# Kernel optimization log

Measured on AMD Instinct MI355X. Metric: run time of the kernel, lower is better.

Reference implementation:

```python
import jax, jax.numpy as jnp
import numpy as np


def setup_inputs() -> dict:
    key = jax.random.key(0)
    ks = jax.random.split(key, 8)
    H, O, B, T = 1024, 512, 512, 256
    s_ih = 1.0 / np.sqrt(H)
    return {
        "h0": jax.random.normal(ks[0], (1, B, H), jnp.float32),
        "c0": jax.random.normal(ks[1], (1, B, H), jnp.float32),
        "W_ih": jax.random.normal(ks[2], (4 * H, O), jnp.float32) * s_ih,
        "W_hh": jax.random.normal(ks[3], (4 * H, H), jnp.float32) * s_ih,
        "b_ih": jax.random.normal(ks[4], (4 * H,), jnp.float32) * s_ih,
        "b_hh": jax.random.normal(ks[5], (4 * H,), jnp.float32) * s_ih,
        "W_out": jax.random.normal(ks[6], (O, H), jnp.float32) * s_ih,
        "b_out": jax.random.normal(ks[7], (O,), jnp.float32) * s_ih,
        "out_len": T,
    }


def reference(h0, c0, W_ih, W_hh, b_ih, b_hh, W_out, b_out, out_len):
    B = h0.shape[1]
    O = W_out.shape[0]
    h = h0.reshape(B, -1)  # [B, H]
    c = c0.reshape(B, -1)  # [B, H]
    x = jnp.zeros((B, O), dtype=h.dtype)  # initial lstm_in of zeros

    def step(carry, _):
        h, c, x = carry
        # PyTorch LSTMCell: gates ordered (i, f, g, o)
        gates = x @ W_ih.T + b_ih + h @ W_hh.T + b_hh  # [B, 4H]
        i, f, g, o = jnp.split(gates, 4, axis=-1)
        c_new = jax.nn.sigmoid(f) * c + jax.nn.sigmoid(i) * jnp.tanh(g)
        h_new = jax.nn.sigmoid(o) * jnp.tanh(c_new)
        y = jax.nn.softmax(h_new @ W_out.T + b_out, axis=-1)  # [B, O]
        return (h_new, c_new, y), y

    _, ys = jax.lax.scan(step, (h, c, x), None, length=out_len)
    # original writes output[i-1] for i = out_len..1, i.e. time-reversed storage
    return ys[::-1]  # [out_len, B, O]
```

## Files before the change

### kernel.cpp

```cpp
#include <hip/hip_runtime.h>
#include <math.h>

#define BB 512
#define HH 1024
#define OO 512
#define KC 1536
#define G4H 4096
#define TT 256

typedef _Float16 half8 __attribute__((ext_vector_type(8)));
typedef float f32x4 __attribute__((ext_vector_type(4)));

__device__ __forceinline__ void dma16(const void* g, void* l) {
    __builtin_amdgcn_global_load_lds(
        (const __attribute__((address_space(1))) void*)g,
        (__attribute__((address_space(3))) void*)l, 16, 0, 0);
}

__global__ __launch_bounds__(256) void conv_wcat(
    const float* __restrict__ W_ih, const float* __restrict__ W_hh,
    _Float16* __restrict__ Wcat)
{
    int k = blockIdx.x * 256 + threadIdx.x;
    int p = blockIdx.y;
    int g = (p >> 5) & 3, jt = p >> 7, jr = p & 31;
    int n = g * HH + jt * 32 + jr;
    float v = (k < OO) ? W_ih[(size_t)n * OO + k] : W_hh[(size_t)n * HH + (k - OO)];
    Wcat[(size_t)p * KC + k] = (_Float16)v;
}

__global__ __launch_bounds__(256) void conv_wout(
    const float* __restrict__ W_out, _Float16* __restrict__ Wout16)
{
    int k = blockIdx.x * 256 + threadIdx.x;
    int o = blockIdx.y;
    Wout16[(size_t)o * HH + k] = (_Float16)W_out[(size_t)o * HH + k];
}

__global__ __launch_bounds__(256) void prep_misc(
    const float* __restrict__ b_ih, const float* __restrict__ b_hh,
    const float* __restrict__ h0, const float* __restrict__ c0,
    float* __restrict__ bias_p, _Float16* __restrict__ xh0, float* __restrict__ cst)
{
    int idx0 = blockIdx.x * blockDim.x + threadIdx.x;
    int stride = gridDim.x * blockDim.x;
    for (int p = idx0; p < G4H; p += stride) {
        int g = (p >> 5) & 3, jt = p >> 7, jr = p & 31;
        int n = g * HH + jt * 32 + jr;
        bias_p[p] = b_ih[n] + b_hh[n];
    }
    for (int i = idx0; i < BB * KC; i += stride) {
        int b = i / KC, q = i - b * KC;
        xh0[i] = (q < OO) ? (_Float16)0.f : (_Float16)h0[b * HH + (q - OO)];
    }
    for (int i = idx0; i < BB * HH; i += stride) cst[i] = c0[i];
}

__global__ __launch_bounds__(256) void gates_mfma(
    const _Float16* __restrict__ xh_in,
    _Float16* __restrict__ xh_out,
    float* __restrict__ cst,
    const _Float16* __restrict__ Wcat,
    const float* __restrict__ bias_p)
{
    const int pt = blockIdx.x;
    const int p0 = pt * 128, b0 = blockIdx.y * 64;
    const int tid = threadIdx.x;
    const int l = tid & 63, w = tid >> 6;
    const int wm = w & 1, wn = w >> 1;
    const int l15 = l & 15, l4 = l >> 4;
    const int lo3 = l & 7;

    __shared__ __align__(16) char smem[49152];
    _Float16* Af = (_Float16*)smem;
    _Float16* Bf = (_Float16*)(smem + 16384);

    f32x4 acc[2][4];
    #pragma unroll
    for (int fm = 0; fm < 2; ++fm)
        #pragma unroll
        for (int fn = 0; fn < 4; ++fn)
            acc[fm][fn] = (f32x4){0.f, 0.f, 0.f, 0.f};

    for (int k0 = 0; k0 < KC; k0 += 128) {
        #pragma unroll
        for (int j = 0; j < 4; ++j) {
            int r0 = (w * 4 + j) * 4;
            int row = r0 + l4;
            int c = (l15) ^ (row & 7);
            dma16(&xh_in[(size_t)(b0 + row) * KC + k0 + c * 8],
                  &Af[(size_t)(w * 4 + j) * 512]);
        }
        #pragma unroll
        for (int j = 0; j < 8; ++j) {
            int r0 = (w * 8 + j) * 4;
            int row = r0 + l4;
            int c = (l15) ^ (row & 7);
            dma16(&Wcat[(size_t)(p0 + row) * KC + k0 + c * 8],
                  &Bf[(size_t)(w * 8 + j) * 512]);
        }
        __syncthreads();

        #pragma unroll
        for (int ks = 0; ks < 4; ++ks) {
            int cc = (ks * 4 + l4) ^ lo3;
            half8 af[2], bf[4];
            #pragma unroll
            for (int fm = 0; fm < 2; ++fm) {
                int R = wm * 32 + fm * 16 + l15;
                af[fm] = *(const half8*)&Af[R * 128 + cc * 8];
            }
            #pragma unroll
            for (int fn = 0; fn < 4; ++fn) {
                int S = wn * 64 + fn * 16 + l15;
                bf[fn] = *(const half8*)&Bf[S * 128 + cc * 8];
            }
            #pragma unroll
            for (int fm = 0; fm < 2; ++fm)
                #pragma unroll
                for (int fn = 0; fn < 4; ++fn)
                    acc[fm][fn] = __builtin_amdgcn_mfma_f32_16x16x32_f16(
                        af[fm], bf[fn], acc[fm][fn], 0, 0, 0);
        }
        __syncthreads();
    }

    float* exch = (float*)smem;
    #pragma unroll
    for (int fm = 0; fm < 2; ++fm)
        #pragma unroll
        for (int fn = 0; fn < 4; ++fn)
            #pragma unroll
            for (int r = 0; r < 4; ++r) {
                int row = wm * 32 + fm * 16 + l4 * 4 + r;
                int col = wn * 64 + fn * 16 + l15;
                exch[row * 133 + col] = acc[fm][fn][r];
            }
    __syncthreads();

    int bl = tid >> 2;
    int b = b0 + bl;
    int jbase = (tid & 3) * 8;
    float cv[8], hv[8];
    float cold[8];
    *(float4*)&cold[0] = *(const float4*)&cst[(size_t)b * HH + pt * 32 + jbase];
    *(float4*)&cold[4] = *(const float4*)&cst[(size_t)b * HH + pt * 32 + jbase + 4];
    #pragma unroll
    for (int u = 0; u < 8; ++u) {
        int jr = jbase + u;
        float gi = exch[bl * 133 +       jr] + bias_p[p0 +       jr];
        float gf = exch[bl * 133 + 32 + jr] + bias_p[p0 + 32 + jr];
        float gg = exch[bl * 133 + 64 + jr] + bias_p[p0 + 64 + jr];
        float go = exch[bl * 133 + 96 + jr] + bias_p[p0 + 96 + jr];
        float iv = 1.f / (1.f + expf(-gi));
        float fv = 1.f / (1.f + expf(-gf));
        float gv = tanhf(gg);
        float ov = 1.f / (1.f + expf(-go));
        float cnew = fv * cold[u] + iv * gv;
        cv[u] = cnew;
        hv[u] = ov * tanhf(cnew);
    }
    *(float4*)&cst[(size_t)b * HH + pt * 32 + jbase]     = *(const float4*)&cv[0];
    *(float4*)&cst[(size_t)b * HH + pt * 32 + jbase + 4] = *(const float4*)&cv[4];
    half8 hh;
    #pragma unroll
    for (int u = 0; u < 8; ++u) hh[u] = (_Float16)hv[u];
    *(half8*)&xh_out[(size_t)b * KC + OO + pt * 32 + jbase] = hh;
}

__global__ __launch_bounds__(128) void logits_mfma(
    const _Float16* __restrict__ xh,
    const _Float16* __restrict__ Wout16,
    const float* __restrict__ b_out,
    float* __restrict__ logits)
{
    const int o0 = blockIdx.x * 32, b0 = blockIdx.y * 32;
    const int tid = threadIdx.x;
    const int l = tid & 63, w = tid >> 6;
    const int l15 = l & 15, l4 = l >> 4, lo3 = l & 7;

    __shared__ __align__(16) _Float16 Ah[32 * 128];
    __shared__ __align__(16) _Float16 Bo[32 * 128];

    f32x4 acc[2];
    acc[0] = (f32x4){0.f, 0.f, 0.f, 0.f};
    acc[1] = (f32x4){0.f, 0.f, 0.f, 0.f};

    for (int k0 = 0; k0 < HH; k0 += 128) {
        #pragma unroll
        for (int j = 0; j < 4; ++j) {
            int row = (w * 4 + j) * 4 + l4;
            int c = l15 ^ (row & 7);
            dma16(&xh[(size_t)(b0 + row) * KC + OO + k0 + c * 8],
                  &Ah[(size_t)(w * 4 + j) * 512]);
        }
        #pragma unroll
        for (int j = 0; j < 4; ++j) {
            int row = (w * 4 + j) * 4 + l4;
            int c = l15 ^ (row & 7);
            dma16(&Wout16[(size_t)(o0 + row) * HH + k0 + c * 8],
                  &Bo[(size_t)(w * 4 + j) * 512]);
        }
        __syncthreads();
        #pragma unroll
        for (int ks = 0; ks < 4; ++ks) {
            int cc = (ks * 4 + l4) ^ lo3;
            int R = w * 16 + l15;
            half8 a = *(const half8*)&Ah[R * 128 + cc * 8];
            #pragma unroll
            for (int fn = 0; fn < 2; ++fn) {
                int S = fn * 16 + l15;
                half8 bq = *(const half8*)&Bo[S * 128 + cc * 8];
                acc[fn] = __builtin_amdgcn_mfma_f32_16x16x32_f16(a, bq, acc[fn], 0, 0, 0);
            }
        }
        __syncthreads();
    }
    #pragma unroll
    for (int fn = 0; fn < 2; ++fn)
        #pragma unroll
        for (int r = 0; r < 4; ++r) {
            int row = b0 + w * 16 + l4 * 4 + r;
            int col = o0 + fn * 16 + l15;
            logits[(size_t)row * OO + col] = acc[fn][r] + b_out[col];
        }
}

__global__ __launch_bounds__(256) void softmax_kernel(
    const float* __restrict__ logits,
    float* __restrict__ out_slice, _Float16* __restrict__ xh_next)
{
    const int w = threadIdx.x >> 6, l = threadIdx.x & 63;
    const int b = blockIdx.x * 4 + w;
    float v[8];
    *(float4*)&v[0] = *(const float4*)&logits[(size_t)b * OO + l * 8];
    *(float4*)&v[4] = *(const float4*)&logits[(size_t)b * OO + l * 8 + 4];

    float m = v[0];
    #pragma unroll
    for (int u = 1; u < 8; ++u) m = fmaxf(m, v[u]);
    #pragma unroll
    for (int off = 1; off < 64; off <<= 1) m = fmaxf(m, __shfl_xor(m, off, 64));

    float s = 0.f;
    #pragma unroll
    for (int u = 0; u < 8; ++u) { v[u] = expf(v[u] - m); s += v[u]; }
    #pragma unroll
    for (int off = 1; off < 64; off <<= 1) s += __shfl_xor(s, off, 64);

    float inv = 1.f / s;
    float y[8];
    half8 hh;
    #pragma unroll
    for (int u = 0; u < 8; ++u) { y[u] = v[u] * inv; hh[u] = (_Float16)y[u]; }
    *(float4*)&out_slice[(size_t)b * OO + l * 8]     = *(const float4*)&y[0];
    *(float4*)&out_slice[(size_t)b * OO + l * 8 + 4] = *(const float4*)&y[4];
    *(half8*)&xh_next[(size_t)b * KC + l * 8] = hh;
}

extern "C" void kernel_launch(void* const* d_in, const int* in_sizes, int n_in,
                              void* d_out, int out_size, void* d_ws, size_t ws_size,
                              hipStream_t stream)
{
    const float* h0    = (const float*)d_in[0];
    const float* c0    = (const float*)d_in[1];
    const float* W_ih  = (const float*)d_in[2];
    const float* W_hh  = (const float*)d_in[3];
    const float* b_ih  = (const float*)d_in[4];
    const float* b_hh  = (const float*)d_in[5];
    const float* W_out = (const float*)d_in[6];
    const float* b_out = (const float*)d_in[7];
    float* out = (float*)d_out;

    char* wsb = (char*)d_ws;
    _Float16* Wcat   = (_Float16*)wsb;                 wsb += (size_t)G4H * KC * 2;
    _Float16* Wout16 = (_Float16*)wsb;                 wsb += (size_t)OO * HH * 2;
    float*    bias_p = (float*)wsb;                    wsb += (size_t)G4H * 4;
    _Float16* xh0    = (_Float16*)wsb;                 wsb += (size_t)BB * KC * 2;
    _Float16* xh1    = (_Float16*)wsb;                 wsb += (size_t)BB * KC * 2;
    float*    cst    = (float*)wsb;                    wsb += (size_t)BB * HH * 4;
    float*    logits = (float*)wsb;                    wsb += (size_t)BB * OO * 4;

    conv_wcat<<<dim3(KC / 256, G4H), 256, 0, stream>>>(W_ih, W_hh, Wcat);
    conv_wout<<<dim3(HH / 256, OO), 256, 0, stream>>>(W_out, Wout16);
    prep_misc<<<512, 256, 0, stream>>>(b_ih, b_hh, h0, c0, bias_p, xh0, cst);

    for (int t = 0; t < TT; ++t) {
        _Float16* xin  = (t & 1) ? xh1 : xh0;
        _Float16* xout = (t & 1) ? xh0 : xh1;
        gates_mfma<<<dim3(32, 8), 256, 0, stream>>>(xin, xout, cst, Wcat, bias_p);
        logits_mfma<<<dim3(16, 16), 128, 0, stream>>>(xout, Wout16, b_out, logits);
        softmax_kernel<<<128, 256, 0, stream>>>(
            logits, out + (size_t)(TT - 1 - t) * BB * OO, xout);
    }
}
```

Before: 8.078 ms.

## Fuse logits GEMM with softmax, pre-swizzle W_out, remap gates blocks per XCD

Merges the per-step logits GEMM and softmax into one kernel. Each block handles 16 batch rows across all 512 outputs, keeps the logits in LDS and removes the global logits round trip and one launch per step. W_out is pre-laid-out in MFMA fragment order so B operands are loaded straight from global memory without LDS staging. The gates grid is flattened and remapped so blocks sharing a weight tile land on the same XCD for L2 reuse. The trade-off is that the fused kernel runs only 32 blocks, which may underuse the GPU's CUs.

```diff
diff --git a/kernel.cpp b/kernel.cpp
--- a/kernel.cpp
+++ b/kernel.cpp
@@ -30,11 +30,15 @@
 }
 
 __global__ __launch_bounds__(256) void conv_wout(
-    const float* __restrict__ W_out, _Float16* __restrict__ Wout16)
+    const float* __restrict__ W_out, _Float16* __restrict__ Woutb)
 {
     int k = blockIdx.x * 256 + threadIdx.x;
     int o = blockIdx.y;
-    Wout16[(size_t)o * HH + k] = (_Float16)W_out[(size_t)o * HH + k];
+    int of = o >> 4, kf = k >> 5;
+    int lidx = ((k >> 3) & 3) * 16 + (o & 15);
+    int u = k & 7;
+    Woutb[((size_t)(of * 32 + kf) << 9) + lidx * 8 + u] =
+        (_Float16)W_out[(size_t)o * HH + k];
 }
 
 __global__ __launch_bounds__(256) void prep_misc(
@@ -63,13 +67,15 @@
     const _Float16* __restrict__ Wcat,
     const float* __restrict__ bias_p)
 {
-    const int pt = blockIdx.x;
-    const int p0 = pt * 128, b0 = blockIdx.y * 64;
+    const int lb = blockIdx.x;
+    const int xcd = lb & 7, idx = lb >> 3;
+    const int pt = xcd * 4 + (idx & 3);
+    const int bt = idx >> 2;
+    const int p0 = pt * 128, b0 = bt * 64;
     const int tid = threadIdx.x;
     const int l = tid & 63, w = tid >> 6;
     const int wm = w & 1, wn = w >> 1;
     const int l15 = l & 15, l4 = l >> 4;
-    const int lo3 = l & 7;
 
     __shared__ __align__(16) char smem[49152];
     _Float16* Af = (_Float16*)smem;
@@ -87,7 +93,7 @@
         for (int j = 0; j < 4; ++j) {
             int r0 = (w * 4 + j) * 4;
             int row = r0 + l4;
-            int c = (l15) ^ (row & 7);
+            int c = l15 ^ (row & 7);
             dma16(&xh_in[(size_t)(b0 + row) * KC + k0 + c * 8],
                   &Af[(size_t)(w * 4 + j) * 512]);
         }
@@ -95,7 +101,7 @@
         for (int j = 0; j < 8; ++j) {
             int r0 = (w * 8 + j) * 4;
             int row = r0 + l4;
-            int c = (l15) ^ (row & 7);
+            int c = l15 ^ (row & 7);
             dma16(&Wcat[(size_t)(p0 + row) * KC + k0 + c * 8],
                   &Bf[(size_t)(w * 8 + j) * 512]);
         }
@@ -103,8 +109,8 @@
 
         #pragma unroll
         for (int ks = 0; ks < 4; ++ks) {
-            int cc = (ks * 4 + l4) ^ lo3;
-            half8 af[2], bf[4];
+            int cc = (ks * 4 + l4) ^ (l15 & 7);
+            half8 af[2], bfr[4];
             #pragma unroll
             for (int fm = 0; fm < 2; ++fm) {
                 int R = wm * 32 + fm * 16 + l15;
@@ -113,14 +119,14 @@
             #pragma unroll
             for (int fn = 0; fn < 4; ++fn) {
                 int S = wn * 64 + fn * 16 + l15;
-                bf[fn] = *(const half8*)&Bf[S * 128 + cc * 8];
+                bfr[fn] = *(const half8*)&Bf[S * 128 + cc * 8];
             }
             #pragma unroll
             for (int fm = 0; fm < 2; ++fm)
                 #pragma unroll
                 for (int fn = 0; fn < 4; ++fn)
                     acc[fm][fn] = __builtin_amdgcn_mfma_f32_16x16x32_f16(
-                        af[fm], bf[fn], acc[fm][fn], 0, 0, 0);
+                        af[fm], bfr[fn], acc[fm][fn], 0, 0, 0);
         }
         __syncthreads();
     }
@@ -141,8 +147,7 @@
     int bl = tid >> 2;
     int b = b0 + bl;
     int jbase = (tid & 3) * 8;
-    float cv[8], hv[8];
-    float cold[8];
+    float cv[8], hv[8], cold[8];
     *(float4*)&cold[0] = *(const float4*)&cst[(size_t)b * HH + pt * 32 + jbase];
     *(float4*)&cold[4] = *(const float4*)&cst[(size_t)b * HH + pt * 32 + jbase + 4];
     #pragma unroll
@@ -168,94 +173,86 @@
     *(half8*)&xh_out[(size_t)b * KC + OO + pt * 32 + jbase] = hh;
 }
 
-__global__ __launch_bounds__(128) void logits_mfma(
+__global__ __launch_bounds__(512) void logits_softmax(
     const _Float16* __restrict__ xh,
-    const _Float16* __restrict__ Wout16,
+    const _Float16* __restrict__ Woutb,
     const float* __restrict__ b_out,
-    float* __restrict__ logits)
-{
-    const int o0 = blockIdx.x * 32, b0 = blockIdx.y * 32;
+    float* __restrict__ out_slice,
+    _Float16* __restrict__ xh_next)
+{
+    const int b0 = blockIdx.x * 16;
     const int tid = threadIdx.x;
     const int l = tid & 63, w = tid >> 6;
-    const int l15 = l & 15, l4 = l >> 4, lo3 = l & 7;
-
-    __shared__ __align__(16) _Float16 Ah[32 * 128];
-    __shared__ __align__(16) _Float16 Bo[32 * 128];
-
-    f32x4 acc[2];
-    acc[0] = (f32x4){0.f, 0.f, 0.f, 0.f};
-    acc[1] = (f32x4){0.f, 0.f, 0.f, 0.f};
-
-    for (int k0 = 0; k0 < HH; k0 += 128) {
-        #pragma unroll
-        for (int j = 0; j < 4; ++j) {
-            int row = (w * 4 + j) * 4 + l4;
-            int c = l15 ^ (row & 7);
-            dma16(&xh[(size_t)(b0 + row) * KC + OO + k0 + c * 8],
-                  &Ah[(size_t)(w * 4 + j) * 512]);
-        }
-        #pragma unroll
-        for (int j = 0; j < 4; ++j) {
-            int row = (w * 4 + j) * 4 + l4;
-            int c = l15 ^ (row & 7);
-            dma16(&Wout16[(size_t)(o0 + row) * HH + k0 + c * 8],
-                  &Bo[(size_t)(w * 4 + j) * 512]);
-        }
-        __syncthreads();
-        #pragma unroll
-        for (int ks = 0; ks < 4; ++ks) {
-            int cc = (ks * 4 + l4) ^ lo3;
-            int R = w * 16 + l15;
-            half8 a = *(const half8*)&Ah[R * 128 + cc * 8];
-            #pragma unroll
-            for (int fn = 0; fn < 2; ++fn) {
-                int S = fn * 16 + l15;
-                half8 bq = *(const half8*)&Bo[S * 128 + cc * 8];
-                acc[fn] = __builtin_amdgcn_mfma_f32_16x16x32_f16(a, bq, acc[fn], 0, 0, 0);
-            }
-        }
-        __syncthreads();
-    }
-    #pragma unroll
-    for (int fn = 0; fn < 2; ++fn)
+    const int l15 = l & 15, l4 = l >> 4;
+
+    __shared__ __align__(16) char smem[33280];
+    _Float16* Ast = (_Float16*)smem;
+
+    #pragma unroll
+    for (int rep = 0; rep < 4; ++rep) {
+        int idxc = rep * 512 + tid;
+        int r = idxc >> 7, c = idxc & 127;
+        half8 v = *(const half8*)&xh[(size_t)(b0 + r) * KC + OO + c * 8];
+        int sl = c ^ (r & 7);
+        *(half8*)&Ast[r * 1024 + sl * 8] = v;
+    }
+    __syncthreads();
+
+    f32x4 acc[4];
+    #pragma unroll
+    for (int fn = 0; fn < 4; ++fn) acc[fn] = (f32x4){0.f, 0.f, 0.f, 0.f};
+
+    #pragma unroll 2
+    for (int kf = 0; kf < 32; ++kf) {
+        int cc = (kf * 4 + l4) ^ (l15 & 7);
+        half8 a = *(const half8*)&Ast[l15 * 1024 + cc * 8];
+        #pragma unroll
+        for (int fn = 0; fn < 4; ++fn) {
+            int of = w * 4 + fn;
+            half8 bq = *(const half8*)&Woutb[((size_t)(of * 32 + kf) << 9) + l * 8];
+            acc[fn] = __builtin_amdgcn_mfma_f32_16x16x32_f16(a, bq, acc[fn], 0, 0, 0);
+        }
+    }
+
+    __syncthreads();
+    float* exch = (float*)smem;
+    #pragma unroll
+    for (int fn = 0; fn < 4; ++fn) {
+        float bo = b_out[w * 64 + fn * 16 + l15];
         #pragma unroll
         for (int r = 0; r < 4; ++r) {
-            int row = b0 + w * 16 + l4 * 4 + r;
-            int col = o0 + fn * 16 + l15;
-            logits[(size_t)row * OO + col] = acc[fn][r] + b_out[col];
-        }
-}
-
-__global__ __launch_bounds__(256) void softmax_kernel(
-    const float* __restrict__ logits,
-    float* __restrict__ out_slice, _Float16* __restrict__ xh_next)
-{
-    const int w = threadIdx.x >> 6, l = threadIdx.x & 63;
-    const int b = blockIdx.x * 4 + w;
-    float v[8];
-    *(float4*)&v[0] = *(const float4*)&logits[(size_t)b * OO + l * 8];
-    *(float4*)&v[4] = *(const float4*)&logits[(size_t)b * OO + l * 8 + 4];
-
-    float m = v[0];
-    #pragma unroll
-    for (int u = 1; u < 8; ++u) m = fmaxf(m, v[u]);
-    #pragma unroll
-    for (int off = 1; off < 64; off <<= 1) m = fmaxf(m, __shfl_xor(m, off, 64));
-
-    float s = 0.f;
-    #pragma unroll
-    for (int u = 0; u < 8; ++u) { v[u] = expf(v[u] - m); s += v[u]; }
-    #pragma unroll
-    for (int off = 1; off < 64; off <<= 1) s += __shfl_xor(s, off, 64);
-
-    float inv = 1.f / s;
-    float y[8];
-    half8 hh;
-    #pragma unroll
-    for (int u = 0; u < 8; ++u) { y[u] = v[u] * inv; hh[u] = (_Float16)y[u]; }
-    *(float4*)&out_slice[(size_t)b * OO + l * 8]     = *(const float4*)&y[0];
-    *(float4*)&out_slice[(size_t)b * OO + l * 8 + 4] = *(const float4*)&y[4];
-    *(half8*)&xh_next[(size_t)b * KC + l * 8] = hh;
+            int row = l4 * 4 + r;
+            int col = w * 64 + fn * 16 + l15;
+            exch[row * 516 + col] = acc[fn][r] + bo;
+        }
+    }
+    __syncthreads();
+
+    #pragma unroll
+    for (int q = 0; q < 2; ++q) {
+        int rr = w * 2 + q;
+        float v[8];
+        *(float4*)&v[0] = *(const float4*)&exch[rr * 516 + l * 8];
+        *(float4*)&v[4] = *(const float4*)&exch[rr * 516 + l * 8 + 4];
+        float m = v[0];
+        #pragma unroll
+        for (int u = 1; u < 8; ++u) m = fmaxf(m, v[u]);
+        #pragma unroll
+        for (int off = 1; off < 64; off <<= 1) m = fmaxf(m, __shfl_xor(m, off, 64));
+        float s = 0.f;
+        #pragma unroll
+        for (int u = 0; u < 8; ++u) { v[u] = expf(v[u] - m); s += v[u]; }
+        #pragma unroll
+        for (int off = 1; off < 64; off <<= 1) s += __shfl_xor(s, off, 64);
+        float inv = 1.f / s;
+        float y[8];
+        half8 hh;
+        #pragma unroll
+        for (int u = 0; u < 8; ++u) { y[u] = v[u] * inv; hh[u] = (_Float16)y[u]; }
+        *(float4*)&out_slice[(size_t)(b0 + rr) * OO + l * 8]     = *(const float4*)&y[0];
+        *(float4*)&out_slice[(size_t)(b0 + rr) * OO + l * 8 + 4] = *(const float4*)&y[4];
+        *(half8*)&xh_next[(size_t)(b0 + rr) * KC + l * 8] = hh;
+    }
 }
 
 extern "C" void kernel_launch(void* const* d_in, const int* in_sizes, int n_in,
@@ -274,23 +271,21 @@
 
     char* wsb = (char*)d_ws;
     _Float16* Wcat   = (_Float16*)wsb;                 wsb += (size_t)G4H * KC * 2;
-    _Float16* Wout16 = (_Float16*)wsb;                 wsb += (size_t)OO * HH * 2;
+    _Float16* Woutb  = (_Float16*)wsb;                 wsb += (size_t)OO * HH * 2;
     float*    bias_p = (float*)wsb;                    wsb += (size_t)G4H * 4;
     _Float16* xh0    = (_Float16*)wsb;                 wsb += (size_t)BB * KC * 2;
     _Float16* xh1    = (_Float16*)wsb;                 wsb += (size_t)BB * KC * 2;
     float*    cst    = (float*)wsb;                    wsb += (size_t)BB * HH * 4;
-    float*    logits = (float*)wsb;                    wsb += (size_t)BB * OO * 4;
 
     conv_wcat<<<dim3(KC / 256, G4H), 256, 0, stream>>>(W_ih, W_hh, Wcat);
-    conv_wout<<<dim3(HH / 256, OO), 256, 0, stream>>>(W_out, Wout16);
+    conv_wout<<<dim3(HH / 256, OO), 256, 0, stream>>>(W_out, Woutb);
     prep_misc<<<512, 256, 0, stream>>>(b_ih, b_hh, h0, c0, bias_p, xh0, cst);
 
     for (int t = 0; t < TT; ++t) {
         _Float16* xin  = (t & 1) ? xh1 : xh0;
         _Float16* xout = (t & 1) ? xh0 : xh1;
-        gates_mfma<<<dim3(32, 8), 256, 0, stream>>>(xin, xout, cst, Wcat, bias_p);
-        logits_mfma<<<dim3(16, 16), 128, 0, stream>>>(xout, Wout16, b_out, logits);
-        softmax_kernel<<<128, 256, 0, stream>>>(
-            logits, out + (size_t)(TT - 1 - t) * BB * OO, xout);
-    }
-}
+        gates_mfma<<<256, 256, 0, stream>>>(xin, xout, cst, Wcat, bias_p);
+        logits_softmax<<<32, 512, 0, stream>>>(
+            xout, Woutb, b_out, out + (size_t)(TT - 1 - t) * BB * OO, xout);
+    }
+}
```

New measurement: 14.72 ms. 1.82x slower.

## Prefetch next K tile into registers to overlap global loads with MFMA

Applied to the files above, without the earlier changes.

Replaces the direct global-to-LDS DMA loads in the gates GEMM with register staging. The next K slice is loaded into registers while MFMAs run on the current LDS tile, then written to LDS after a barrier. The aim is to hide global load latency behind compute without adding a second LDS buffer. The cost is extra VGPRs for the 12 staged half8 vectors and an extra LDS write pass, which may lower occupancy.

```diff
diff --git a/kernel.cpp b/kernel.cpp
--- a/kernel.cpp
+++ b/kernel.cpp
@@ -69,7 +69,6 @@
     const int l = tid & 63, w = tid >> 6;
     const int wm = w & 1, wn = w >> 1;
     const int l15 = l & 15, l4 = l >> 4;
-    const int lo3 = l & 7;
 
     __shared__ __align__(16) char smem[49152];
     _Float16* Af = (_Float16*)smem;
@@ -82,29 +81,43 @@
         for (int fn = 0; fn < 4; ++fn)
             acc[fm][fn] = (f32x4){0.f, 0.f, 0.f, 0.f};
 
-    for (int k0 = 0; k0 < KC; k0 += 128) {
+    half8 ra[4], rb[8];
+
+    auto load_regs = [&](int k0) {
         #pragma unroll
         for (int j = 0; j < 4; ++j) {
-            int r0 = (w * 4 + j) * 4;
-            int row = r0 + l4;
-            int c = (l15) ^ (row & 7);
-            dma16(&xh_in[(size_t)(b0 + row) * KC + k0 + c * 8],
-                  &Af[(size_t)(w * 4 + j) * 512]);
+            int row = (w * 4 + j) * 4 + l4;
+            int c = l15 ^ (row & 7);
+            ra[j] = *(const half8*)&xh_in[(size_t)(b0 + row) * KC + k0 + c * 8];
         }
         #pragma unroll
         for (int j = 0; j < 8; ++j) {
-            int r0 = (w * 8 + j) * 4;
-            int row = r0 + l4;
-            int c = (l15) ^ (row & 7);
-            dma16(&Wcat[(size_t)(p0 + row) * KC + k0 + c * 8],
-                  &Bf[(size_t)(w * 8 + j) * 512]);
-        }
+            int row = (w * 8 + j) * 4 + l4;
+            int c = l15 ^ (row & 7);
+            rb[j] = *(const half8*)&Wcat[(size_t)(p0 + row) * KC + k0 + c * 8];
+        }
+    };
+    auto store_lds = [&]() {
+        #pragma unroll
+        for (int j = 0; j < 4; ++j)
+            *(half8*)&Af[(size_t)(w * 4 + j) * 512 + l * 8] = ra[j];
+        #pragma unroll
+        for (int j = 0; j < 8; ++j)
+            *(half8*)&Bf[(size_t)(w * 8 + j) * 512 + l * 8] = rb[j];
+    };
+
+    load_regs(0);
+    #pragma unroll 1
+    for (int it = 0; it < KC / 128; ++it) {
         __syncthreads();
+        store_lds();
+        __syncthreads();
+        if (it + 1 < KC / 128) load_regs((it + 1) * 128);
 
         #pragma unroll
         for (int ks = 0; ks < 4; ++ks) {
-            int cc = (ks * 4 + l4) ^ lo3;
-            half8 af[2], bf[4];
+            int cc = (ks * 4 + l4) ^ (l15 & 7);
+            half8 af[2], bfr[4];
             #pragma unroll
             for (int fm = 0; fm < 2; ++fm) {
                 int R = wm * 32 + fm * 16 + l15;
@@ -113,17 +126,17 @@
             #pragma unroll
             for (int fn = 0; fn < 4; ++fn) {
                 int S = wn * 64 + fn * 16 + l15;
-                bf[fn] = *(const half8*)&Bf[S * 128 + cc * 8];
+                bfr[fn] = *(const half8*)&Bf[S * 128 + cc * 8];
             }
             #pragma unroll
             for (int fm = 0; fm < 2; ++fm)
                 #pragma unroll
                 for (int fn = 0; fn < 4; ++fn)
                     acc[fm][fn] = __builtin_amdgcn_mfma_f32_16x16x32_f16(
-                        af[fm], bf[fn], acc[fm][fn], 0, 0, 0);
-        }
-        __syncthreads();
-    }
+                        af[fm], bfr[fn], acc[fm][fn], 0, 0, 0);
+        }
+    }
+    __syncthreads();
 
     float* exch = (float*)smem;
     #pragma unroll
@@ -141,8 +154,7 @@
     int bl = tid >> 2;
     int b = b0 + bl;
     int jbase = (tid & 3) * 8;
-    float cv[8], hv[8];
-    float cold[8];
+    float cv[8], hv[8], cold[8];
     *(float4*)&cold[0] = *(const float4*)&cst[(size_t)b * HH + pt * 32 + jbase];
     *(float4*)&cold[4] = *(const float4*)&cst[(size_t)b * HH + pt * 32 + jbase + 4];
     #pragma unroll
```

Result: faster. 7.311 ms (-9.5%).
